# Kernel tuning notes

Measured on AMD Instinct MI355X. Metric: run time of the kernel, lower is better.

Reference implementation:

```python
import jax, jax.numpy as jnp
from jax import lax
import numpy as np

N_SPLITS = 2
N_LEVELS = 3
B, T, C = 32, 1024, 128
HID = 512          # int(input_dim * hidden_size) = 128 * 4
K1, K2 = 5, 3      # first conv kernel_size, second conv kernel=3
N_INTER = 7        # 1 + 2 + 4 interactors in the binary tree
LEAKY_SLOPE = 0.01


def setup_inputs() -> dict:
    key = jax.random.key(0)
    ks = jax.random.split(key, 9)
    w = 0.05  # small init so exp-gating stays well-conditioned
    return {
        "x": jax.random.normal(ks[0], (B, T, C), jnp.float32),
        "mul_w1": jax.random.normal(ks[1], (N_INTER, N_SPLITS, K1, C, HID), jnp.float32) * w,
        "mul_b1": jnp.zeros((N_INTER, N_SPLITS, HID), jnp.float32),
        "mul_w2": jax.random.normal(ks[2], (N_INTER, N_SPLITS, K2, HID, C), jnp.float32) * w,
        "mul_b2": jnp.zeros((N_INTER, N_SPLITS, C), jnp.float32),
        "add_w1": jax.random.normal(ks[3], (N_INTER, N_SPLITS, K1, C, HID), jnp.float32) * w,
        "add_b1": jnp.zeros((N_INTER, N_SPLITS, HID), jnp.float32),
        "add_w2": jax.random.normal(ks[4], (N_INTER, N_SPLITS, K2, HID, C), jnp.float32) * w,
        "add_b2": jnp.zeros((N_INTER, N_SPLITS, C), jnp.float32),
    }


def _leaky(x):
    return jnp.where(x > 0, x, LEAKY_SLOPE * x)


def _causal_conv(x, w, b):
    # x: [B, L, Cin], w: [K, Cin, Cout] (keras WIO layout); 'causal' = left-pad K-1
    k = w.shape[0]
    y = lax.conv_general_dilated(x, w, window_strides=(1,),
                                 padding=[(k - 1, 0)],
                                 dimension_numbers=("NWC", "WIO", "NWC"))
    return y + b


def _conv_seq(x, w1, b1, w2, b2):
    # Conv1D(causal, LeakyReLU 0.01) -> Dropout(identity at inference) -> Conv1D(k=3, causal, tanh)
    h = _leaky(_causal_conv(x, w1, b1))
    return jnp.tanh(_causal_conv(h, w2, b2))


def _interactor(x, idx, p):
    # x: [B, L, C]; strided temporal split into N_SPLITS pieces of length L//N_SPLITS
    splits = [x[:, i::N_SPLITS, :] for i in range(N_SPLITS)]
    scale = N_SPLITS - 1
    mul_list = []
    for i in range(N_SPLITS):
        s = 0.0
        for j in range(N_SPLITS):
            if j != i:
                s = s + _conv_seq(splits[j], p["mul_w1"][idx, i], p["mul_b1"][idx, i],
                                  p["mul_w2"][idx, i], p["mul_b2"][idx, i])
        # prod_j exp(f(x_j)) ** (1/scale) == exp(sum_j f(x_j) / scale)
        mul_list.append(splits[i] * jnp.exp(s / scale))
    out = []
    for i in range(N_SPLITS):
        a = 0.0
        for j in range(N_SPLITS):
            if j != i:
                a = a + _conv_seq(mul_list[j], p["add_w1"][idx, i], p["add_b1"][idx, i],
                                  p["add_w2"][idx, i], p["add_b2"][idx, i])
        a = a / scale
        out.append(mul_list[i] + a if i % 2 == 0 else mul_list[i] - a)
    return out


def reference(x, mul_w1, mul_b1, mul_w2, mul_b2, add_w1, add_b1, add_w2, add_b2):
    p = {"mul_w1": mul_w1, "mul_b1": mul_b1, "mul_w2": mul_w2, "mul_b2": mul_b2,
         "add_w1": add_w1, "add_b1": add_b1, "add_w2": add_w2, "add_b2": add_b2}
    t_in = x.shape[1]
    min_unit = N_SPLITS ** N_LEVELS
    pad = (-t_in) % min_unit  # left zero-pad to a multiple of n_splits**n_levels
    xp = jnp.pad(x, ((0, 0), (pad, 0), (0, 0)))
    seq = [xp]
    idx = 0
    for lvl in range(N_LEVELS):
        nxt = []
        for j in range(N_SPLITS ** lvl):
            nxt += _interactor(seq[j], idx, p)
            idx += 1
        seq = nxt
    # rev_split: recursively concatenate along time with stride `steps`
    while len(seq) > 1:
        steps = len(seq) // N_SPLITS
        seq = [jnp.concatenate([seq[i + s * steps] for s in range(N_SPLITS)], axis=1)
               for i in range(steps)]
    return seq[0][:, -t_in:, :]
```

## Files before the change

### kernel.cpp

```cpp
#include <hip/hip_runtime.h>
#include <hip/hip_bf16.h>
#include <stdint.h>


static constexpr int B_ = 32, T_ = 1024, C_ = 128, HID_ = 512;
static constexpr int K1_ = 5, K2_ = 3;

typedef __attribute__((ext_vector_type(8))) _Float16 half8;
typedef __attribute__((ext_vector_type(4))) float f32x4;

__device__ __forceinline__ unsigned short f2h(float f) {
    _Float16 h = (_Float16)f;
    return __builtin_bit_cast(unsigned short, h);
}

__device__ __forceinline__ void gload16(const void* g, void* l) {
    __builtin_amdgcn_global_load_lds(
        (const __attribute__((address_space(1))) unsigned int*)g,
        (__attribute__((address_space(3))) unsigned int*)l, 16, 0, 0);
}

template<int CIN, int COUT>
__global__ __launch_bounds__(256)
void wprep_k(const float* __restrict__ win1, unsigned short* __restrict__ wout1,
             const float* __restrict__ win2, unsigned short* __restrict__ wout2,
             int nhalf) {
    constexpr int TA = CIN / 64, TB = COUT / 64;
    int blk = blockIdx.x;
    int tb = blk % TB;
    int ta = (blk / TB) % TA;
    int s  = blk / (TA * TB);
    const float* win;
    unsigned short* wout;
    if (s < nhalf) { win = win1; wout = wout1; }
    else           { win = win2; wout = wout2; s -= nhalf; }
    __shared__ float tile[64][65];
    const float* src = win + (size_t)s * CIN * COUT;
    unsigned short* dst = wout + (size_t)s * CIN * COUT;
    int cl = threadIdx.x & 63;
    int rw = threadIdx.x >> 6;
    for (int r = rw; r < 64; r += 4)
        tile[r][cl] = src[(size_t)(ta * 64 + r) * COUT + tb * 64 + cl];
    __syncthreads();
    for (int r = rw; r < 64; r += 4) {
        int co = tb * 64 + r;
        int ci = ta * 64 + cl;
        int ciw = (ci & ~127) | ((ci & 127) ^ ((co & 7) << 3));
        dst[(size_t)co * CIN + ciw] = f2h(tile[cl][r]);
    }
}

__global__ __launch_bounds__(256)
void split_k(const float* __restrict__ cur, unsigned short* __restrict__ outb,
             int Ls) {
    int idx = blockIdx.x * 256 + threadIdx.x;
    int row = idx >> 5;
    int cq  = (idx & 31) << 2;
    int BLs = B_ * Ls;
    int g  = row / BLs;
    int r2 = row - g * BLs;
    int b  = r2 / Ls;
    int u  = r2 - b * Ls;
    int p = g >> 1, i = g & 1;
    const float4 v = *(const float4*)(cur +
        ((size_t)(p * B_ + b) * (2 * Ls) + 2 * u + i) * C_ + cq);
    ushort4 o;
    o.x = f2h(v.x); o.y = f2h(v.y); o.z = f2h(v.z); o.w = f2h(v.w);
    int cqw = cq ^ (((u + 4) & 7) << 3);
    *(ushort4*)(outb + (size_t)row * C_ + cqw) = o;
}

__global__ __launch_bounds__(256, 2)
void conv1_k(const unsigned short* __restrict__ actb,
             const unsigned short* __restrict__ wT,
             const float* __restrict__ bias,
             unsigned short* __restrict__ hid,
             const unsigned short* __restrict__ zp,
             int Ls, int RT, int idxbase) {
    __shared__ unsigned short smemA[132 * 128];
    __shared__ unsigned short smemB[128 * 128];

    const int tid = threadIdx.x;
    const int lane = tid & 63;
    const int w = tid >> 6;
    const int wr = w >> 1, wc = w & 1;

    int blk = blockIdx.x;
    const int ct2 = blk & 1;
    int t1 = blk >> 1;
    const int rt = t1 % RT;
    const int g  = t1 / RT;
    const int rowstart = rt * 128;
    const int b  = rowstart / Ls;
    const int t0 = rowstart - b * Ls;

    const int gin  = g ^ 1;
    const int widx = (idxbase + (g >> 1)) * 2 + (g & 1);

    const char* inb = (const char*)(actb + (size_t)(gin * B_ + b) * Ls * C_);
    const char* wb  = (const char*)(wT + (size_t)widx * (K1_ * HID_ * C_));
    const float* bptr = bias + (size_t)widx * HID_;

    for (int ch = w; ch < 33; ch += 4) {
        int q = ch * 1024 + lane * 16;
        int r = q >> 8;
        int cb = q & 255;
        int t = t0 - 4 + r;
        const char* src = (t >= 0) ? inb + (size_t)t * 256 + cb
                                   : (const char*)zp + cb;
        gload16(src, (char*)smemA + ch * 1024);
    }

    unsigned short* outp = hid + ((size_t)(g * B_ + b) * Ls + t0) * HID_;

    for (int ctl = 0; ctl < 2; ++ctl) {
        const int n0 = (ct2 * 2 + ctl) * 128;

        f32x4 acc[4][4];
#pragma unroll
        for (int m = 0; m < 4; ++m)
#pragma unroll
            for (int n = 0; n < 4; ++n) acc[m][n] = (f32x4){0.f, 0.f, 0.f, 0.f};

        for (int kk = 0; kk < K1_; ++kk) {
            if (ctl | kk) __syncthreads();
            const char* wt = wb + (size_t)kk * HID_ * C_ * 2;
            for (int ch = w; ch < 32; ch += 4) {
                int q = ch * 1024 + lane * 16;
                int co = q >> 8;
                int cb = q & 255;
                gload16(wt + (size_t)(n0 + co) * 256 + cb, (char*)smemB + ch * 1024);
            }
            asm volatile("s_waitcnt vmcnt(0)" ::: "memory");
            __syncthreads();

#pragma unroll
            for (int ks = 0; ks < 4; ++ks) {
                half8 aF[4], bF[4];
                const int cole = ks * 32 + ((lane >> 4) << 3);
#pragma unroll
                for (int m = 0; m < 4; ++m) {
                    int ar = kk + wr * 64 + m * 16 + (lane & 15);
                    aF[m] = *(const half8*)(smemA + ar * 128 + (cole ^ ((ar & 7) << 3)));
                }
#pragma unroll
                for (int n = 0; n < 4; ++n) {
                    int br = wc * 64 + n * 16 + (lane & 15);
                    bF[n] = *(const half8*)(smemB + br * 128 + (cole ^ ((br & 7) << 3)));
                }
#pragma unroll
                for (int m = 0; m < 4; ++m)
#pragma unroll
                    for (int n = 0; n < 4; ++n)
                        acc[m][n] = __builtin_amdgcn_mfma_f32_16x16x32_f16(
                            aF[m], bF[n], acc[m][n], 0, 0, 0);
            }
        }

#pragma unroll
        for (int n = 0; n < 4; ++n) {
            int co = n0 + wc * 64 + n * 16 + (lane & 15);
            float bv = bptr[co];
#pragma unroll
            for (int m = 0; m < 4; ++m) {
                int u0 = wr * 64 + m * 16 + ((lane >> 4) << 2);
#pragma unroll
                for (int q = 0; q < 4; ++q) {
                    float v = acc[m][n][q] + bv;
                    v = (v > 0.f) ? v : 0.01f * v;
                    int t = t0 + u0 + q;
                    int cow = (co & ~127) | ((co & 127) ^ (((t + 2) & 7) << 3));
                    outp[(size_t)(u0 + q) * HID_ + cow] = f2h(v);
                }
            }
        }
    }
}

template<int EPI>
__global__ __launch_bounds__(256, 2)
void conv2_k(const unsigned short* __restrict__ hid,
             const unsigned short* __restrict__ wT,
             const float* __restrict__ bias,
             const float* __restrict__ cur,
             float* __restrict__ mulf,
             unsigned short* __restrict__ actb,
             float* __restrict__ nxt,
             unsigned short* __restrict__ actn,
             float* __restrict__ dout,
             const unsigned short* __restrict__ zp,
             int Ls, int RT, int idxbase) {
    __shared__ unsigned short smemA[66 * 128];
    __shared__ unsigned short smemB[128 * 128];

    const int tid = threadIdx.x;
    const int lane = tid & 63;
    const int w = tid >> 6;
    const int wr = w >> 1, wc = w & 1;

    int blk = blockIdx.x;
    const int rt = blk % RT;
    const int g  = blk / RT;
    const int rowstart = rt * 64;
    const int b  = rowstart / Ls;
    const int t0 = rowstart - b * Ls;
    const int widx = (idxbase + (g >> 1)) * 2 + (g & 1);

    const char* inb = (const char*)(hid + (size_t)(g * B_ + b) * Ls * HID_);
    const char* wb  = (const char*)(wT + (size_t)widx * (K2_ * C_ * HID_));
    const float* bptr = bias + (size_t)widx * C_;

    f32x4 acc[2][4];
#pragma unroll
    for (int m = 0; m < 2; ++m)
#pragma unroll
        for (int n = 0; n < 4; ++n) acc[m][n] = (f32x4){0.f, 0.f, 0.f, 0.f};

    for (int ck = 0; ck < 4; ++ck) {
        if (ck) __syncthreads();
        for (int ch = w; ch < 17; ch += 4) {
            int q = ch * 1024 + lane * 16;
            if (q < 16896) {
                int r = q >> 8;
                int cb = q & 255;
                int t = t0 - 2 + r;
                const char* src = (t >= 0)
                    ? inb + (size_t)t * 1024 + ck * 256 + cb
                    : (const char*)zp + cb;
                gload16(src, (char*)smemA + ch * 1024);
            }
        }
        for (int kk = 0; kk < K2_; ++kk) {
            if (kk) __syncthreads();
            const char* wt = wb + (size_t)kk * C_ * HID_ * 2;
            for (int ch = w; ch < 32; ch += 4) {
                int q = ch * 1024 + lane * 16;
                int co = q >> 8;
                int cb = q & 255;
                gload16(wt + (size_t)co * 1024 + ck * 256 + cb,
                        (char*)smemB + ch * 1024);
            }
            asm volatile("s_waitcnt vmcnt(0)" ::: "memory");
            __syncthreads();

#pragma unroll
            for (int ks = 0; ks < 4; ++ks) {
                half8 aF[2], bF[4];
                const int cole = ks * 32 + ((lane >> 4) << 3);
#pragma unroll
                for (int m = 0; m < 2; ++m) {
                    int ar = kk + wr * 32 + m * 16 + (lane & 15);
                    aF[m] = *(const half8*)(smemA + ar * 128 + (cole ^ ((ar & 7) << 3)));
                }
#pragma unroll
                for (int n = 0; n < 4; ++n) {
                    int br = wc * 64 + n * 16 + (lane & 15);
                    bF[n] = *(const half8*)(smemB + br * 128 + (cole ^ ((br & 7) << 3)));
                }
#pragma unroll
                for (int m = 0; m < 2; ++m)
#pragma unroll
                    for (int n = 0; n < 4; ++n)
                        acc[m][n] = __builtin_amdgcn_mfma_f32_16x16x32_f16(
                            aF[m], bF[n], acc[m][n], 0, 0, 0);
            }
        }
    }

    const size_t rowb = (size_t)(g * B_ + b) * Ls + t0;
    const int p_ = g >> 1, i_ = g & 1;
    const int Ls2 = Ls >> 1;
#pragma unroll
    for (int n = 0; n < 4; ++n) {
        int c = wc * 64 + n * 16 + (lane & 15);
        float bv = bptr[c];
#pragma unroll
        for (int m = 0; m < 2; ++m) {
            int u0 = wr * 32 + m * 16 + ((lane >> 4) << 2);
#pragma unroll
            for (int q = 0; q < 4; ++q) {
                float v = acc[m][n][q] + bv;
                float xc = fminf(fmaxf(v, -15.f), 15.f);
                float e2 = __expf(2.f * xc);
                float th = (e2 - 1.f) / (e2 + 1.f);
                size_t ro = rowb + (size_t)(u0 + q);
                int u = t0 + u0 + q;
                if (EPI == 0) {
                    float sv = cur[((size_t)(p_ * B_ + b) * (2 * Ls) + 2 * u + i_) * C_ + c];
                    float mv = sv * __expf(th);
                    mulf[ro * C_ + c] = mv;
                    int cw = c ^ (((u + 4) & 7) << 3);
                    actb[ro * C_ + cw] = f2h(mv);
                } else {
                    float mv = mulf[ro * C_ + c];
                    float val = (i_ == 0) ? (mv + th) : (mv - th);
                    if (EPI == 1) {
                        nxt[ro * C_ + c] = val;
                        int gq = g * 2 + (u & 1);
                        int uq = u >> 1;
                        int cw = c ^ (((uq + 4) & 7) << 3);
                        actn[((size_t)(gq * B_ + b) * Ls2 + uq) * C_ + cw] = f2h(val);
                    } else {
                        int tau = u | (((g >> 2) & 1) << 7) | (((g >> 1) & 1) << 8)
                                    | ((g & 1) << 9);
                        dout[((size_t)b * T_ + tau) * C_ + c] = val;
                    }
                }
            }
        }
    }
}

extern "C" void kernel_launch(void* const* d_in, const int* in_sizes, int n_in,
                              void* d_out, int out_size, void* d_ws, size_t ws_size,
                              hipStream_t stream) {
    const float* x   = (const float*)d_in[0];
    const float* mw1 = (const float*)d_in[1];
    const float* mb1 = (const float*)d_in[2];
    const float* mw2 = (const float*)d_in[3];
    const float* mb2 = (const float*)d_in[4];
    const float* aw1 = (const float*)d_in[5];
    const float* ab1 = (const float*)d_in[6];
    const float* aw2 = (const float*)d_in[7];
    const float* ab2 = (const float*)d_in[8];

    char* ws = (char*)d_ws;
    size_t off = 0;
    auto alloc = [&](size_t sz) {
        char* p = ws + off;
        off += (sz + 255) & ~(size_t)255;
        return p;
    };
    unsigned short* zp   = (unsigned short*)alloc(8192);
    unsigned short* w1m  = (unsigned short*)alloc((size_t)14 * 5 * 512 * 128 * 2);
    unsigned short* w1a  = (unsigned short*)alloc((size_t)14 * 5 * 512 * 128 * 2);
    unsigned short* w2m  = (unsigned short*)alloc((size_t)14 * 3 * 128 * 512 * 2);
    unsigned short* w2a  = (unsigned short*)alloc((size_t)14 * 3 * 128 * 512 * 2);
    float* bufA          = (float*)alloc((size_t)4194304 * 4);
    float* bufB          = (float*)alloc((size_t)4194304 * 4);
    unsigned short* actb = (unsigned short*)alloc((size_t)4194304 * 2);
    unsigned short* hidb = (unsigned short*)alloc((size_t)16777216 * 2);
    float* mulf          = (float*)alloc((size_t)4194304 * 4);
    (void)ws_size; (void)n_in; (void)in_sizes; (void)out_size;

    hipMemsetAsync(zp, 0, 8192, stream);

    wprep_k<128, 512><<<2240, 256, 0, stream>>>(mw1, w1m, aw1, w1a, 70);
    wprep_k<512, 128><<<1344, 256, 0, stream>>>(mw2, w2m, aw2, w2a, 42);

    split_k<<<4096, 256, 0, stream>>>(x, actb, 512);

    for (int lvl = 0; lvl < 3; ++lvl) {
        const int P = 1 << lvl;
        const int G = 2 * P;
        const int Ls = (1024 >> lvl) >> 1;
        const int idxbase = P - 1;
        const float* cur = (lvl == 0) ? x : ((lvl == 1) ? bufA : bufB);
        float* nxt = (lvl == 1) ? bufB : bufA;
        const int RT1 = Ls / 4;
        const int RT2 = Ls / 2;

        conv1_k<<<G * RT1 * 2, 256, 0, stream>>>(actb, w1m, mb1, hidb, zp,
                                                 Ls, RT1, idxbase);
        conv2_k<0><<<G * RT2, 256, 0, stream>>>(hidb, w2m, mb2, cur, mulf,
                                                actb, nullptr, nullptr, nullptr,
                                                zp, Ls, RT2, idxbase);
        conv1_k<<<G * RT1 * 2, 256, 0, stream>>>(actb, w1a, ab1, hidb, zp,
                                                 Ls, RT1, idxbase);
        if (lvl < 2) {
            conv2_k<1><<<G * RT2, 256, 0, stream>>>(hidb, w2a, ab2, nullptr, mulf,
                                                    nullptr, nxt, actb, nullptr,
                                                    zp, Ls, RT2, idxbase);
        } else {
            conv2_k<2><<<G * RT2, 256, 0, stream>>>(hidb, w2a, ab2, nullptr, mulf,
                                                    nullptr, nullptr, nullptr,
                                                    (float*)d_out,
                                                    zp, Ls, RT2, idxbase);
        }
    }
}
```

Baseline: 394.3 us.

## Fuse both causal convs into one kernel keeping hidden activations in LDS

```diff
diff --git a/kernel.cpp b/kernel.cpp
--- a/kernel.cpp
+++ b/kernel.cpp
@@ -66,203 +66,152 @@
         ((size_t)(p * B_ + b) * (2 * Ls) + 2 * u + i) * C_ + cq);
     ushort4 o;
     o.x = f2h(v.x); o.y = f2h(v.y); o.z = f2h(v.z); o.w = f2h(v.w);
-    int cqw = cq ^ (((u + 4) & 7) << 3);
+    int cqw = cq ^ ((u & 7) << 3);
     *(ushort4*)(outb + (size_t)row * C_ + cqw) = o;
 }
 
-__global__ __launch_bounds__(256, 2)
-void conv1_k(const unsigned short* __restrict__ actb,
-             const unsigned short* __restrict__ wT,
-             const float* __restrict__ bias,
-             unsigned short* __restrict__ hid,
+template<int EPI>
+__global__ __launch_bounds__(512, 1)
+void fused_k(const unsigned short* __restrict__ ain,
+             const unsigned short* __restrict__ w1,
+             const unsigned short* __restrict__ w2,
+             const float* __restrict__ b1,
+             const float* __restrict__ b2,
+             const float* __restrict__ cur,
+             float* __restrict__ mulf,
+             unsigned short* __restrict__ aout,
+             float* __restrict__ nxt,
+             unsigned short* __restrict__ actn,
+             float* __restrict__ dout,
              const unsigned short* __restrict__ zp,
-             int Ls, int RT, int idxbase) {
-    __shared__ unsigned short smemA[132 * 128];
-    __shared__ unsigned short smemB[128 * 128];
+             int Ls, int TPG, int idxbase) {
+    __shared__ unsigned short aIn[144 * 128];
+    __shared__ unsigned short hidT[136 * 128];
+    __shared__ unsigned short wbuf[128 * 128];
 
     const int tid = threadIdx.x;
     const int lane = tid & 63;
     const int w = tid >> 6;
     const int wr = w >> 1, wc = w & 1;
-
-    int blk = blockIdx.x;
-    const int ct2 = blk & 1;
-    int t1 = blk >> 1;
-    const int rt = t1 % RT;
-    const int g  = t1 / RT;
-    const int rowstart = rt * 128;
-    const int b  = rowstart / Ls;
-    const int t0 = rowstart - b * Ls;
-
+    const int hi8 = (lane >> 4) << 3;
+    const int l15 = lane & 15;
+
+    const int blk = blockIdx.x;
+    const int g    = blk / TPG;
+    const int tile = blk % TPG;
+    const int b  = (tile * 128) / Ls;
+    const int t0 = (tile * 128) % Ls;
     const int gin  = g ^ 1;
     const int widx = (idxbase + (g >> 1)) * 2 + (g & 1);
 
-    const char* inb = (const char*)(actb + (size_t)(gin * B_ + b) * Ls * C_);
-    const char* wb  = (const char*)(wT + (size_t)widx * (K1_ * HID_ * C_));
-    const float* bptr = bias + (size_t)widx * HID_;
-
-    for (int ch = w; ch < 33; ch += 4) {
+    const char* ain_g = (const char*)(ain + (size_t)(gin * B_ + b) * Ls * C_);
+    const char* w1b = (const char*)(w1 + (size_t)widx * (K1_ * HID_ * C_));
+    const char* w2b = (const char*)(w2 + (size_t)widx * (K2_ * C_ * HID_));
+
+    const int bco = lane >> 4;
+    const int bcb = l15 * 16;
+
+    for (int ch = w; ch < 36; ch += 8) {
         int q = ch * 1024 + lane * 16;
-        int r = q >> 8;
+        int ur = q >> 8;
         int cb = q & 255;
-        int t = t0 - 4 + r;
-        const char* src = (t >= 0) ? inb + (size_t)t * 256 + cb
+        int u = t0 - 8 + ur;
+        const char* src = (u >= 0) ? ain_g + (size_t)u * 256 + cb
                                    : (const char*)zp + cb;
-        gload16(src, (char*)smemA + ch * 1024);
-    }
-
-    unsigned short* outp = hid + ((size_t)(g * B_ + b) * Ls + t0) * HID_;
-
-    for (int ctl = 0; ctl < 2; ++ctl) {
-        const int n0 = (ct2 * 2 + ctl) * 128;
-
-        f32x4 acc[4][4];
-#pragma unroll
-        for (int m = 0; m < 4; ++m)
-#pragma unroll
-            for (int n = 0; n < 4; ++n) acc[m][n] = (f32x4){0.f, 0.f, 0.f, 0.f};
-
-        for (int kk = 0; kk < K1_; ++kk) {
-            if (ctl | kk) __syncthreads();
-            const char* wt = wb + (size_t)kk * HID_ * C_ * 2;
-            for (int ch = w; ch < 32; ch += 4) {
-                int q = ch * 1024 + lane * 16;
-                int co = q >> 8;
-                int cb = q & 255;
-                gload16(wt + (size_t)(n0 + co) * 256 + cb, (char*)smemB + ch * 1024);
+        gload16(src, (char*)aIn + ch * 1024);
+    }
+
+    f32x4 acc2[2][4];
+#pragma unroll
+    for (int m = 0; m < 2; ++m)
+#pragma unroll
+        for (int n = 0; n < 4; ++n) acc2[m][n] = (f32x4){0.f, 0.f, 0.f, 0.f};
+
+    for (int ck = 0; ck < 4; ++ck) {
+        f32x4 acc1[3][4];
+#pragma unroll
+        for (int ti = 0; ti < 3; ++ti)
+#pragma unroll
+            for (int n = 0; n < 4; ++n) acc1[ti][n] = (f32x4){0.f, 0.f, 0.f, 0.f};
+
+        for (int tap = 0; tap < K1_; ++tap) {
+            __syncthreads();
+#pragma unroll
+            for (int j = 0; j < 4; ++j) {
+                int ch = w * 4 + j;
+                gload16(w1b + (size_t)(tap * HID_ + ck * 128 + ch * 4 + bco) * 256 + bcb,
+                        (char*)wbuf + ch * 1024);
             }
             asm volatile("s_waitcnt vmcnt(0)" ::: "memory");
             __syncthreads();
 
 #pragma unroll
-            for (int ks = 0; ks < 4; ++ks) {
-                half8 aF[4], bF[4];
-                const int cole = ks * 32 + ((lane >> 4) << 3);
-#pragma unroll
-                for (int m = 0; m < 4; ++m) {
-                    int ar = kk + wr * 64 + m * 16 + (lane & 15);
-                    aF[m] = *(const half8*)(smemA + ar * 128 + (cole ^ ((ar & 7) << 3)));
+            for (int ti = 0; ti < 3; ++ti) {
+                if (ti == 2 && wr != 3) continue;
+                const int moff = (ti < 2) ? (wr * 32 + ti * 16) : 114;
+                const int ai = moff + l15 + tap + 2;
+#pragma unroll
+                for (int ks = 0; ks < 4; ++ks) {
+                    half8 aF = *(const half8*)(aIn + ai * 128
+                        + ((ks * 32 + hi8) ^ ((ai & 7) << 3)));
+#pragma unroll
+                    for (int n = 0; n < 4; ++n) {
+                        int co = wc * 64 + n * 16 + l15;
+                        half8 bF = *(const half8*)(wbuf + co * 128
+                            + ((ks * 32 + hi8) ^ ((co & 7) << 3)));
+                        acc1[ti][n] = __builtin_amdgcn_mfma_f32_16x16x32_f16(
+                            aF, bF, acc1[ti][n], 0, 0, 0);
+                    }
                 }
-#pragma unroll
-                for (int n = 0; n < 4; ++n) {
-                    int br = wc * 64 + n * 16 + (lane & 15);
-                    bF[n] = *(const half8*)(smemB + br * 128 + (cole ^ ((br & 7) << 3)));
+            }
+        }
+
+#pragma unroll
+        for (int ti = 0; ti < 3; ++ti) {
+            if (ti == 2 && wr != 3) continue;
+            const int moff = (ti < 2) ? (wr * 32 + ti * 16) : 114;
+#pragma unroll
+            for (int n = 0; n < 4; ++n) {
+                int c = wc * 64 + n * 16 + l15;
+                float bv = b1[(size_t)widx * HID_ + ck * 128 + c];
+#pragma unroll
+                for (int q = 0; q < 4; ++q) {
+                    int r = moff + ((lane >> 4) << 2) + q;
+                    float v = acc1[ti][n][q] + bv;
+                    v = (v > 0.f) ? v : 0.01f * v;
+                    hidT[r * 128 + (c ^ ((r & 7) << 3))] = f2h(v);
                 }
-#pragma unroll
-                for (int m = 0; m < 4; ++m)
-#pragma unroll
-                    for (int n = 0; n < 4; ++n)
-                        acc[m][n] = __builtin_amdgcn_mfma_f32_16x16x32_f16(
-                            aF[m], bF[n], acc[m][n], 0, 0, 0);
-            }
-        }
-
-#pragma unroll
-        for (int n = 0; n < 4; ++n) {
-            int co = n0 + wc * 64 + n * 16 + (lane & 15);
-            float bv = bptr[co];
-#pragma unroll
-            for (int m = 0; m < 4; ++m) {
-                int u0 = wr * 64 + m * 16 + ((lane >> 4) << 2);
-#pragma unroll
-                for (int q = 0; q < 4; ++q) {
-                    float v = acc[m][n][q] + bv;
-                    v = (v > 0.f) ? v : 0.01f * v;
-                    int t = t0 + u0 + q;
-                    int cow = (co & ~127) | ((co & 127) ^ (((t + 2) & 7) << 3));
-                    outp[(size_t)(u0 + q) * HID_ + cow] = f2h(v);
-                }
-            }
-        }
-    }
-}
-
-template<int EPI>
-__global__ __launch_bounds__(256, 2)
-void conv2_k(const unsigned short* __restrict__ hid,
-             const unsigned short* __restrict__ wT,
-             const float* __restrict__ bias,
-             const float* __restrict__ cur,
-             float* __restrict__ mulf,
-             unsigned short* __restrict__ actb,
-             float* __restrict__ nxt,
-             unsigned short* __restrict__ actn,
-             float* __restrict__ dout,
-             const unsigned short* __restrict__ zp,
-             int Ls, int RT, int idxbase) {
-    __shared__ unsigned short smemA[66 * 128];
-    __shared__ unsigned short smemB[128 * 128];
-
-    const int tid = threadIdx.x;
-    const int lane = tid & 63;
-    const int w = tid >> 6;
-    const int wr = w >> 1, wc = w & 1;
-
-    int blk = blockIdx.x;
-    const int rt = blk % RT;
-    const int g  = blk / RT;
-    const int rowstart = rt * 64;
-    const int b  = rowstart / Ls;
-    const int t0 = rowstart - b * Ls;
-    const int widx = (idxbase + (g >> 1)) * 2 + (g & 1);
-
-    const char* inb = (const char*)(hid + (size_t)(g * B_ + b) * Ls * HID_);
-    const char* wb  = (const char*)(wT + (size_t)widx * (K2_ * C_ * HID_));
-    const float* bptr = bias + (size_t)widx * C_;
-
-    f32x4 acc[2][4];
-#pragma unroll
-    for (int m = 0; m < 2; ++m)
-#pragma unroll
-        for (int n = 0; n < 4; ++n) acc[m][n] = (f32x4){0.f, 0.f, 0.f, 0.f};
-
-    for (int ck = 0; ck < 4; ++ck) {
-        if (ck) __syncthreads();
-        for (int ch = w; ch < 17; ch += 4) {
-            int q = ch * 1024 + lane * 16;
-            if (q < 16896) {
-                int r = q >> 8;
-                int cb = q & 255;
-                int t = t0 - 2 + r;
-                const char* src = (t >= 0)
-                    ? inb + (size_t)t * 1024 + ck * 256 + cb
-                    : (const char*)zp + cb;
-                gload16(src, (char*)smemA + ch * 1024);
-            }
-        }
+            }
+        }
+
         for (int kk = 0; kk < K2_; ++kk) {
-            if (kk) __syncthreads();
-            const char* wt = wb + (size_t)kk * C_ * HID_ * 2;
-            for (int ch = w; ch < 32; ch += 4) {
-                int q = ch * 1024 + lane * 16;
-                int co = q >> 8;
-                int cb = q & 255;
-                gload16(wt + (size_t)co * 1024 + ck * 256 + cb,
-                        (char*)smemB + ch * 1024);
+            __syncthreads();
+#pragma unroll
+            for (int j = 0; j < 4; ++j) {
+                int ch = w * 4 + j;
+                gload16(w2b + (size_t)kk * (C_ * HID_ * 2)
+                            + (size_t)(ch * 4 + bco) * 1024 + ck * 256 + bcb,
+                        (char*)wbuf + ch * 1024);
             }
             asm volatile("s_waitcnt vmcnt(0)" ::: "memory");
             __syncthreads();
 
 #pragma unroll
-            for (int ks = 0; ks < 4; ++ks) {
-                half8 aF[2], bF[4];
-                const int cole = ks * 32 + ((lane >> 4) << 3);
-#pragma unroll
-                for (int m = 0; m < 2; ++m) {
-                    int ar = kk + wr * 32 + m * 16 + (lane & 15);
-                    aF[m] = *(const half8*)(smemA + ar * 128 + (cole ^ ((ar & 7) << 3)));
+            for (int m = 0; m < 2; ++m) {
+                const int ar = wr * 32 + m * 16 + l15 + kk;
+#pragma unroll
+                for (int ks = 0; ks < 4; ++ks) {
+                    half8 aF = *(const half8*)(hidT + ar * 128
+                        + ((ks * 32 + hi8) ^ ((ar & 7) << 3)));
+#pragma unroll
+                    for (int n = 0; n < 4; ++n) {
+                        int co = wc * 64 + n * 16 + l15;
+                        half8 bF = *(const half8*)(wbuf + co * 128
+                            + ((ks * 32 + hi8) ^ ((co & 7) << 3)));
+                        acc2[m][n] = __builtin_amdgcn_mfma_f32_16x16x32_f16(
+                            aF, bF, acc2[m][n], 0, 0, 0);
+                    }
                 }
-#pragma unroll
-                for (int n = 0; n < 4; ++n) {
-                    int br = wc * 64 + n * 16 + (lane & 15);
-                    bF[n] = *(const half8*)(smemB + br * 128 + (cole ^ ((br & 7) << 3)));
-                }
-#pragma unroll
-                for (int m = 0; m < 2; ++m)
-#pragma unroll
-                    for (int n = 0; n < 4; ++n)
-                        acc[m][n] = __builtin_amdgcn_mfma_f32_16x16x32_f16(
-                            aF[m], bF[n], acc[m][n], 0, 0, 0);
             }
         }
     }
@@ -272,14 +221,14 @@
     const int Ls2 = Ls >> 1;
 #pragma unroll
     for (int n = 0; n < 4; ++n) {
-        int c = wc * 64 + n * 16 + (lane & 15);
-        float bv = bptr[c];
+        int c = wc * 64 + n * 16 + l15;
+        float bv = b2[(size_t)widx * C_ + c];
 #pragma unroll
         for (int m = 0; m < 2; ++m) {
             int u0 = wr * 32 + m * 16 + ((lane >> 4) << 2);
 #pragma unroll
             for (int q = 0; q < 4; ++q) {
-                float v = acc[m][n][q] + bv;
+                float v = acc2[m][n][q] + bv;
                 float xc = fminf(fmaxf(v, -15.f), 15.f);
                 float e2 = __expf(2.f * xc);
                 float th = (e2 - 1.f) / (e2 + 1.f);
@@ -289,8 +238,7 @@
                     float sv = cur[((size_t)(p_ * B_ + b) * (2 * Ls) + 2 * u + i_) * C_ + c];
                     float mv = sv * __expf(th);
                     mulf[ro * C_ + c] = mv;
-                    int cw = c ^ (((u + 4) & 7) << 3);
-                    actb[ro * C_ + cw] = f2h(mv);
+                    aout[ro * C_ + (c ^ ((u & 7) << 3))] = f2h(mv);
                 } else {
                     float mv = mulf[ro * C_ + c];
                     float val = (i_ == 0) ? (mv + th) : (mv - th);
@@ -298,8 +246,8 @@
                         nxt[ro * C_ + c] = val;
                         int gq = g * 2 + (u & 1);
                         int uq = u >> 1;
-                        int cw = c ^ (((uq + 4) & 7) << 3);
-                        actn[((size_t)(gq * B_ + b) * Ls2 + uq) * C_ + cw] = f2h(val);
+                        actn[((size_t)(gq * B_ + b) * Ls2 + uq) * C_
+                             + (c ^ ((uq & 7) << 3))] = f2h(val);
                     } else {
                         int tau = u | (((g >> 2) & 1) << 7) | (((g >> 1) & 1) << 8)
                                     | ((g & 1) << 9);
@@ -339,7 +287,7 @@
     float* bufA          = (float*)alloc((size_t)4194304 * 4);
     float* bufB          = (float*)alloc((size_t)4194304 * 4);
     unsigned short* actb = (unsigned short*)alloc((size_t)4194304 * 2);
-    unsigned short* hidb = (unsigned short*)alloc((size_t)16777216 * 2);
+    unsigned short* actg = (unsigned short*)alloc((size_t)4194304 * 2);
     float* mulf          = (float*)alloc((size_t)4194304 * 4);
     (void)ws_size; (void)n_in; (void)in_sizes; (void)out_size;
 
@@ -351,31 +299,28 @@
     split_k<<<4096, 256, 0, stream>>>(x, actb, 512);
 
     for (int lvl = 0; lvl < 3; ++lvl) {
-        const int P = 1 << lvl;
-        const int G = 2 * P;
+        const int G = 2 << lvl;
         const int Ls = (1024 >> lvl) >> 1;
-        const int idxbase = P - 1;
-        const float* cur = (lvl == 0) ? x : ((lvl == 1) ? bufA : bufB);
-        float* nxt = (lvl == 1) ? bufB : bufA;
-        const int RT1 = Ls / 4;
-        const int RT2 = Ls / 2;
-
-        conv1_k<<<G * RT1 * 2, 256, 0, stream>>>(actb, w1m, mb1, hidb, zp,
-                                                 Ls, RT1, idxbase);
-        conv2_k<0><<<G * RT2, 256, 0, stream>>>(hidb, w2m, mb2, cur, mulf,
-                                                actb, nullptr, nullptr, nullptr,
-                                                zp, Ls, RT2, idxbase);
-        conv1_k<<<G * RT1 * 2, 256, 0, stream>>>(actb, w1a, ab1, hidb, zp,
-                                                 Ls, RT1, idxbase);
+        const int idxbase = (1 << lvl) - 1;
+        const float* curp = (lvl == 0) ? x : ((lvl == 1) ? bufA : bufB);
+        float* nxtp = (lvl == 1) ? bufB : bufA;
+        const int TPG = B_ * Ls / 128;
+        const int grid = G * TPG;
+
+        fused_k<0><<<grid, 512, 0, stream>>>(actb, w1m, w2m, mb1, mb2,
+                                             curp, mulf, actg,
+                                             nullptr, nullptr, nullptr,
+                                             zp, Ls, TPG, idxbase);
         if (lvl < 2) {
-            conv2_k<1><<<G * RT2, 256, 0, stream>>>(hidb, w2a, ab2, nullptr, mulf,
-                                                    nullptr, nxt, actb, nullptr,
-                                                    zp, Ls, RT2, idxbase);
+            fused_k<1><<<grid, 512, 0, stream>>>(actg, w1a, w2a, ab1, ab2,
+                                                 nullptr, mulf, nullptr,
+                                                 nxtp, actb, nullptr,
+                                                 zp, Ls, TPG, idxbase);
         } else {
-            conv2_k<2><<<G * RT2, 256, 0, stream>>>(hidb, w2a, ab2, nullptr, mulf,
-                                                    nullptr, nullptr, nullptr,
-                                                    (float*)d_out,
-                                                    zp, Ls, RT2, idxbase);
-        }
-    }
-}
+            fused_k<2><<<grid, 512, 0, stream>>>(actg, w1a, w2a, ab1, ab2,
+                                                 nullptr, mulf, nullptr,
+                                                 nullptr, nullptr, (float*)d_out,
+                                                 zp, Ls, TPG, idxbase);
+        }
+    }
+}
```

Result: slower. 903.6 us (+129.2%).
